# Kernel optimization log

Hardware: AMD Instinct MI355X
Metric: run time of the kernel (lower is better)

Reference implementation:

```python
import jax, jax.numpy as jnp
import numpy as np
from jax import lax

D = 1024      # hidden_dim
H = 1408      # moe_inter_dim
E = 8         # num_experts
K = 2         # topk
ROUTER_SCALE = 1.0


def setup_inputs() -> dict:
    key = jax.random.key(0)
    ks = jax.random.split(key, 16)
    s = 0.02
    inp = {
        "x": jax.random.normal(ks[0], (2, 2048, D), dtype=jnp.float32),
        "gate_w": jax.random.normal(ks[1], (E, D), dtype=jnp.float32) * s,
        "gate_b": jax.random.normal(ks[2], (E,), dtype=jnp.float32) * s,
        # stacked expert params; torch Linear weight [out,in] stored transposed as [in,out]
        "w1": jax.random.normal(ks[3], (E, D, H), dtype=jnp.float32) * s,
        "b1": jax.random.normal(ks[4], (E, H), dtype=jnp.float32) * s,
        "w3": jax.random.normal(ks[5], (E, D, H), dtype=jnp.float32) * s,
        "b3": jax.random.normal(ks[6], (E, H), dtype=jnp.float32) * s,
        "w2": jax.random.normal(ks[7], (E, H, D), dtype=jnp.float32) * s,
        "b2": jax.random.normal(ks[8], (E, D), dtype=jnp.float32) * s,
        # shared expert
        "sw1": jax.random.normal(ks[9], (D, H), dtype=jnp.float32) * s,
        "sb1": jax.random.normal(ks[10], (H,), dtype=jnp.float32) * s,
        "sw3": jax.random.normal(ks[11], (D, H), dtype=jnp.float32) * s,
        "sb3": jax.random.normal(ks[12], (H,), dtype=jnp.float32) * s,
        "sw2": jax.random.normal(ks[13], (H, D), dtype=jnp.float32) * s,
        "sb2": jax.random.normal(ks[14], (D,), dtype=jnp.float32) * s,
    }
    return inp


def _expert(x, w1, b1, w3, b3, w2, b2):
    # NOTE: source applies silu to the PRODUCT: w2(silu(w1(x) * w3(x)))
    h = jax.nn.silu((x @ w1 + b1) * (x @ w3 + b3))
    return h @ w2 + b2


def reference(x, gate_w, gate_b, w1, b1, w3, b3, w2, b2,
              sw1, sb1, sw3, sb3, sw2, sb2):
    shape = x.shape
    xf = x.reshape(-1, D)                      # [T, D]
    T = xf.shape[0]

    # Gate
    scores = jax.nn.softmax(xf @ gate_w.T, axis=-1)   # [T, E]
    biased = scores + gate_b
    _, idx = lax.top_k(biased, K)                     # [T, K] int32
    w = jnp.take_along_axis(scores, idx, axis=-1) * ROUTER_SCALE  # [T, K]

    # Dense routing-weight matrix (top-k indices are distinct per token)
    rw = jnp.zeros((T, E), dtype=xf.dtype).at[jnp.arange(T)[:, None], idx].add(w)

    # Stacked expert compute: [T, E, H] -> [T, E, D], combined by routing weight
    h = jax.nn.silu((jnp.einsum('td,edh->teh', xf, w1) + b1)
                    * (jnp.einsum('td,edh->teh', xf, w3) + b3))
    oe = jnp.einsum('teh,ehd->ted', h, w2) + b2
    y = jnp.einsum('te,ted->td', rw, oe)

    # Shared expert on all tokens
    z = _expert(xf, sw1, sb1, sw3, sb3, sw2, sb2)
    return (y + z).reshape(shape)
```

## Files before the change

### kernel.cpp

```cpp
#include <hip/hip_runtime.h>
#include <math.h>

#define DD 1024
#define HH 1408
#define NE 8

typedef __attribute__((ext_vector_type(8))) __bf16 bf16x8;
typedef __attribute__((ext_vector_type(4))) float f32x4;

__device__ __forceinline__ float bf2f(unsigned short u) {
  union { unsigned int i; float f; } v; v.i = ((unsigned int)u) << 16; return v.f;
}
__device__ __forceinline__ unsigned short f2bf(float f) {
  union { float f; unsigned int i; } v; v.f = f;
  unsigned int r = v.i + 0x7FFFu + ((v.i >> 16) & 1u);
  return (unsigned short)(r >> 16);
}
__device__ __forceinline__ float tof(float f) { return f; }
__device__ __forceinline__ float tof(unsigned short u) { return bf2f(u); }

__device__ __forceinline__ void cvt2(float a, float b, unsigned int* o) {
  asm("v_cvt_pk_bf16_f32 %0, %1, %2" : "=v"(*o) : "v"(a), "v"(b));
}

__device__ __forceinline__ void ld8cvt(const float* p, unsigned int* o) {
  float4 a = *(const float4*)p;
  float4 b = *(const float4*)(p + 4);
  cvt2(a.x, a.y, o + 0); cvt2(a.z, a.w, o + 1);
  cvt2(b.x, b.y, o + 2); cvt2(b.z, b.w, o + 3);
}

typedef unsigned int __attribute__((address_space(1))) gu32;
typedef unsigned int __attribute__((address_space(3))) lu32;
__device__ __forceinline__ void gl16(const unsigned short* g, unsigned short* l) {
  __builtin_amdgcn_global_load_lds((const gu32*)g, (lu32*)l, 16, 0, 0);
}

__global__ void sniff_kernel(const unsigned short* __restrict__ xw,
                             int* __restrict__ dflag) {
  __shared__ int cnt;
  if (threadIdx.x == 0) cnt = 0;
  __syncthreads();
  unsigned short v = xw[threadIdx.x];
  int e = (v >> 7) & 0xFF;
  if (e >= 100 && e <= 140) atomicAdd(&cnt, 1);
  __syncthreads();
  if (threadIdx.x == 0) dflag[0] = (cnt < 230) ? 1 : 0;
}

__global__ void cvtx_kernel(const void* __restrict__ x,
                            const int* __restrict__ dflag,
                            unsigned short* __restrict__ xb, int n8) {
  int i = blockIdx.x * blockDim.x + threadIdx.x;
  int st = gridDim.x * blockDim.x;
  if (dflag[0]) {
    const float* xs = (const float*)x;
    for (; i < n8; i += st) {
      unsigned int o[4];
      ld8cvt(xs + (size_t)i * 8, o);
      *(uint4*)(xb + (size_t)i * 8) = *(uint4*)o;
    }
  } else {
    const uint4* xs = (const uint4*)x;
    for (; i < n8; i += st) *(uint4*)(xb + (size_t)i * 8) = xs[i];
  }
}

__global__ void trans_kernel(const void* __restrict__ wmain,
                             const void* __restrict__ wsh,
                             const int* __restrict__ dflag,
                             unsigned short* __restrict__ out, int R, int C) {
  __shared__ float tile[32][33];
  const int mat = blockIdx.z;
  const int r0 = blockIdx.y << 5, c0 = blockIdx.x << 5;
  const int t = threadIdx.x;
  const int lr = t >> 3, lc = (t & 7) << 2;
  const size_t mbase = (size_t)mat * R * C;
  if (dflag[0]) {
    const float* src = (mat < NE) ? ((const float*)wmain + mbase) : (const float*)wsh;
    float4 v = *(const float4*)(src + (size_t)(r0 + lr) * C + c0 + lc);
    tile[lr][lc] = v.x; tile[lr][lc + 1] = v.y;
    tile[lr][lc + 2] = v.z; tile[lr][lc + 3] = v.w;
  } else {
    const unsigned short* src = (mat < NE) ? ((const unsigned short*)wmain + mbase)
                                           : (const unsigned short*)wsh;
    ushort4 v = *(const ushort4*)(src + (size_t)(r0 + lr) * C + c0 + lc);
    tile[lr][lc] = bf2f(v.x); tile[lr][lc + 1] = bf2f(v.y);
    tile[lr][lc + 2] = bf2f(v.z); tile[lr][lc + 3] = bf2f(v.w);
  }
  __syncthreads();
  const int oc = t >> 3;
  const int orr = (t & 7) << 2;
  unsigned int p0, p1;
  cvt2(tile[orr][oc], tile[orr + 1][oc], &p0);
  cvt2(tile[orr + 2][oc], tile[orr + 3][oc], &p1);
  uint2 pk; pk.x = p0; pk.y = p1;
  *(uint2*)(out + mbase + (size_t)(c0 + oc) * R + r0 + orr) = pk;
}

__global__ void cvtb_kernel(const void* b1, const void* b3, const void* b2,
                            const void* sb1, const void* sb3, const void* sb2,
                            const int* __restrict__ dflag,
                            float* __restrict__ bf1, float* __restrict__ bf3,
                            float* __restrict__ bf2o) {
  int i = blockIdx.x * blockDim.x + threadIdx.x;
  const int nh = (NE + 1) * HH, nd = (NE + 1) * DD;
  const bool f32 = dflag[0] != 0;
  auto get = [&](const void* pm, const void* ps, int idx, int per) -> float {
    int mat = idx / per, j = idx - mat * per;
    if (f32) return (mat < NE) ? ((const float*)pm)[(size_t)mat * per + j]
                               : ((const float*)ps)[j];
    return bf2f((mat < NE) ? ((const unsigned short*)pm)[(size_t)mat * per + j]
                           : ((const unsigned short*)ps)[j]);
  };
  if (i < nh) bf1[i] = get(b1, sb1, i, HH);
  else if (i < 2 * nh) bf3[i - nh] = get(b3, sb3, i - nh, HH);
  else if (i < 2 * nh + nd) bf2o[i - 2 * nh] = get(b2, sb2, i - 2 * nh, DD);
}

template <class T>
__device__ void gate_body(const T* __restrict__ x,
                          const T* __restrict__ gw,
                          const T* __restrict__ gb,
                          int* __restrict__ tok_eidx,
                          float* __restrict__ tok_w, int T_) {
  int t = (int)((blockIdx.x * blockDim.x + threadIdx.x) >> 6);
  int lane = threadIdx.x & 63;
  if (t >= T_) return;
  const T* xr = x + (size_t)t * DD;
  float acc[NE];
#pragma unroll
  for (int e = 0; e < NE; e++) acc[e] = 0.f;
  for (int i = lane; i < DD; i += 64) {
    float xv = tof(xr[i]);
#pragma unroll
    for (int e = 0; e < NE; e++) acc[e] += xv * tof(gw[e * DD + i]);
  }
#pragma unroll
  for (int off = 32; off > 0; off >>= 1) {
#pragma unroll
    for (int e = 0; e < NE; e++) acc[e] += __shfl_xor(acc[e], off);
  }
  if (lane == 0) {
    float mx = acc[0];
#pragma unroll
    for (int e = 1; e < NE; e++) mx = fmaxf(mx, acc[e]);
    float s = 0.f, sc[NE], bi[NE];
#pragma unroll
    for (int e = 0; e < NE; e++) { sc[e] = expf(acc[e] - mx); s += sc[e]; }
    float inv = 1.f / s;
#pragma unroll
    for (int e = 0; e < NE; e++) { sc[e] *= inv; bi[e] = sc[e] + tof(gb[e]); }
    int i1 = 0;
#pragma unroll
    for (int e = 1; e < NE; e++) if (bi[e] > bi[i1]) i1 = e;
    int i2 = (i1 == 0) ? 1 : 0;
#pragma unroll
    for (int e = 0; e < NE; e++) if (e != i1 && bi[e] > bi[i2]) i2 = e;
    tok_eidx[t * 2] = i1; tok_eidx[t * 2 + 1] = i2;
    tok_w[t * 2] = sc[i1]; tok_w[t * 2 + 1] = sc[i2];
  }
}

__global__ void gate_kernel(const void* x, const void* gw, const void* gb,
                            const int* __restrict__ dflag,
                            int* tok_eidx, float* tok_w, int T_) {
  if (dflag[0])
    gate_body<float>((const float*)x, (const float*)gw, (const float*)gb,
                     tok_eidx, tok_w, T_);
  else
    gate_body<unsigned short>((const unsigned short*)x, (const unsigned short*)gw,
                              (const unsigned short*)gb, tok_eidx, tok_w, T_);
}

__global__ void prep_kernel(const int* __restrict__ tok_eidx,
                            const float* __restrict__ tok_w,
                            int* __restrict__ meta,
                            int* __restrict__ rows_tok,
                            float* __restrict__ rows_wgt,
                            int t0, int TS) {
  __shared__ int cnt[NE];
  __shared__ int off[NE];
  const int tid = threadIdx.x;
  if (tid < NE) cnt[tid] = 0;
  __syncthreads();
  const int n2 = TS * 2;
  const int* te = tok_eidx + (size_t)t0 * 2;
  const float* tw = tok_w + (size_t)t0 * 2;
  for (int i = tid; i < n2; i += (int)blockDim.x) atomicAdd(&cnt[te[i]], 1);
  __syncthreads();
  if (tid == 0) {
    int s = 0;
#pragma unroll
    for (int e = 0; e < NE; e++) { off[e] = s; meta[16 + e] = s; s += cnt[e]; }
    meta[16 + NE] = s;
  }
  __syncthreads();
  for (int i = tid; i < n2; i += (int)blockDim.x) {
    int pos = atomicAdd(&off[te[i]], 1);
    rows_tok[pos] = t0 + (i >> 1);
    rows_wgt[pos] = tw[i];
  }
}

__global__ void zero_kernel(float4* __restrict__ p, int n4) {
  int i = blockIdx.x * blockDim.x + threadIdx.x;
  int st = gridDim.x * blockDim.x;
  float4 z; z.x = z.y = z.z = z.w = 0.f;
  for (; i < n4; i += st) p[i] = z;
}

__global__ __launch_bounds__(512, 2)
void ffn_up_kernel(const unsigned short* __restrict__ xb,
                   const unsigned short* __restrict__ wt1,
                   const unsigned short* __restrict__ wt3,
                   const float* __restrict__ bf1, const float* __restrict__ bf3,
                   const int* __restrict__ meta,
                   const int* __restrict__ rows_tok,
                   unsigned short* __restrict__ h_buf,
                   unsigned short* __restrict__ sh_buf,
                   int t0, int TS, int my) {
  const int NX = HH / 128;
  const int P = NX * (NE + 1);
  const int id = blockIdx.x;
  const int xcd = id & 7;
  const int rest = id >> 3;
  const int mtile = rest % my;
  const int chunk = rest / my;
  const int panel = chunk * 8 + xcd;
  if (panel >= P) return;
  const int z = panel / NX;
  const int n0 = (panel - z * NX) * 128;

  const bool shx = (z == NE);
  int g0, cnt;
  unsigned short* ho;
  if (shx) { g0 = 0; cnt = TS; ho = sh_buf; }
  else {
    g0 = meta[16 + z]; cnt = meta[17 + z] - g0;
    ho = h_buf + (size_t)g0 * HH;
  }
  if (mtile * 256 >= cnt) return;
  const unsigned short* wa = wt1 + (size_t)z * HH * DD;
  const unsigned short* wb = wt3 + (size_t)z * HH * DD;

  __shared__ alignas(16) unsigned short lds[2 * 32768];

  const int tid = threadIdx.x;
  const int lane = tid & 63, wid = tid >> 6;
  const int rsub = wid * 8 + (lane >> 3);
  const int sl8 = (((lane & 7) ^ (lane >> 3)) << 3);

  size_t aoff[4];
#pragma unroll
  for (int c = 0; c < 4; c++) {
    int r = c * 64 + rsub;
    int m = mtile * 256 + r;
    int rr = (m < cnt) ? m : (cnt - 1);
    int srow = shx ? (t0 + rr) : rows_tok[g0 + rr];
    aoff[c] = (size_t)srow * DD + sl8;
  }
  size_t boff[2];
#pragma unroll
  for (int c = 0; c < 2; c++)
    boff[c] = (size_t)(n0 + c * 64 + rsub) * DD + sl8;

  const int ln15 = lane & 15;
  const int lg = lane >> 4;
  const int wr = (wid >> 1) << 6;
  const int wc = (wid & 1) << 6;
  const int ldsw = wid * 512;

  f32x4 acc1[4][4], acc3[4][4];
#pragma unroll
  for (int a = 0; a < 4; a++)
#pragma unroll
    for (int b = 0; b < 4; b++) {
      acc1[a][b] = {0.f, 0.f, 0.f, 0.f};
      acc3[a][b] = {0.f, 0.f, 0.f, 0.f};
    }

  auto stage = [&](int buf, int k) {
    unsigned short* Lb = &lds[buf * 32768];
#pragma unroll
    for (int c = 0; c < 4; c++)
      gl16(xb + aoff[c] + k, Lb + c * 4096 + ldsw);
#pragma unroll
    for (int c = 0; c < 2; c++) {
      gl16(wa + boff[c] + k, Lb + 16384 + c * 4096 + ldsw);
      gl16(wb + boff[c] + k, Lb + 24576 + c * 4096 + ldsw);
    }
  };

  stage(0, 0);
  const int NT = DD / 64;
  for (int t = 0; t < NT; ++t) {
    asm volatile("s_waitcnt vmcnt(0)" ::: "memory");
    __syncthreads();
    if (t + 1 < NT) stage((t + 1) & 1, (t + 1) * 64);
    const unsigned short* Lb = &lds[(t & 1) * 32768];
#pragma unroll
    for (int ks = 0; ks < 2; ks++) {
      bf16x8 af[4];
#pragma unroll
      for (int fm = 0; fm < 4; fm++) {
        int R = wr + fm * 16 + ln15;
        af[fm] = *(const bf16x8*)&Lb[R * 64 + ((((ks << 2) | lg) ^ (R & 7)) << 3)];
      }
#pragma unroll
      for (int fn = 0; fn < 4; fn++) {
        int Rb = wc + fn * 16 + ln15;
        int o = Rb * 64 + ((((ks << 2) | lg) ^ (Rb & 7)) << 3);
        bf16x8 b1v = *(const bf16x8*)&Lb[16384 + o];
        bf16x8 b3v = *(const bf16x8*)&Lb[24576 + o];
#pragma unroll
        for (int fm = 0; fm < 4; fm++) {
          acc1[fm][fn] = __builtin_amdgcn_mfma_f32_16x16x32_bf16(af[fm], b1v, acc1[fm][fn], 0, 0, 0);
          acc3[fm][fn] = __builtin_amdgcn_mfma_f32_16x16x32_bf16(af[fm], b3v, acc3[fm][fn], 0, 0, 0);
        }
      }
    }
  }

  const int kq4 = lg << 2;
#pragma unroll
  for (int fm = 0; fm < 4; fm++) {
#pragma unroll
    for (int r = 0; r < 4; r++) {
      int m = mtile * 256 + wr + fm * 16 + kq4 + r;
      if (m < cnt) {
        unsigned short* orow = ho + (size_t)m * HH + n0;
#pragma unroll
        for (int fn = 0; fn < 4; fn++) {
          int nc = wc + fn * 16 + ln15;
          float g1 = acc1[fm][fn][r] + bf1[(size_t)z * HH + n0 + nc];
          float g3 = acc3[fm][fn][r] + bf3[(size_t)z * HH + n0 + nc];
          float u = g1 * g3;
          float hv = u * __builtin_amdgcn_rcpf(1.f + __expf(-u));
          orow[nc] = f2bf(hv);
        }
      }
    }
  }
}

__global__ __launch_bounds__(512, 2)
void ffn_down_kernel(const unsigned short* __restrict__ h_buf,
                     const unsigned short* __restrict__ sh_buf,
                     const unsigned short* __restrict__ wt2,
                     const float* __restrict__ bf2,
                     const int* __restrict__ meta,
                     const int* __restrict__ rows_tok,
                     const float* __restrict__ rows_wgt,
                     float* __restrict__ out, int t0, int TS, int my) {
  const int NX = DD / 128;
  const int P = NX * (NE + 1);
  const int id = blockIdx.x;
  const int xcd = id & 7;
  const int rest = id >> 3;
  const int mtile = rest % my;
  const int chunk = rest / my;
  const int panel = chunk * 8 + xcd;
  if (panel >= P) return;
  const int z = panel / NX;
  const int n0 = (panel - z * NX) * 128;

  const bool shx = (z == NE);
  int g0, cnt;
  const unsigned short* hb;
  if (shx) { g0 = 0; cnt = TS; hb = sh_buf; }
  else {
    g0 = meta[16 + z]; cnt = meta[17 + z] - g0;
    hb = h_buf + (size_t)g0 * HH;
  }
  if (mtile * 256 >= cnt) return;
  const unsigned short* ws = wt2 + (size_t)z * DD * HH;

  __shared__ alignas(16) unsigned short lds[2 * 24576];

  const int tid = threadIdx.x;
  const int lane = tid & 63, wid = tid >> 6;
  const int rsub = wid * 8 + (lane >> 3);
  const int sl8 = (((lane & 7) ^ (lane >> 3)) << 3);

  size_t aoff[4];
#pragma unroll
  for (int c = 0; c < 4; c++) {
    int r = c * 64 + rsub;
    int m = mtile * 256 + r;
    int rr = (m < cnt) ? m : (cnt - 1);
    aoff[c] = (size_t)rr * HH + sl8;
  }
  size_t boff[2];
#pragma unroll
  for (int c = 0; c < 2; c++)
    boff[c] = (size_t)(n0 + c * 64 + rsub) * HH + sl8;

  const int ln15 = lane & 15;
  const int lg = lane >> 4;
  const int wr = (wid >> 1) << 6;
  const int wc = (wid & 1) << 6;
  const int ldsw = wid * 512;

  f32x4 acc[4][4];
#pragma unroll
  for (int a = 0; a < 4; a++)
#pragma unroll
    for (int b = 0; b < 4; b++) acc[a][b] = {0.f, 0.f, 0.f, 0.f};

  auto stage = [&](int buf, int k) {
    unsigned short* Lb = &lds[buf * 24576];
#pragma unroll
    for (int c = 0; c < 4; c++)
      gl16(hb + aoff[c] + k, Lb + c * 4096 + ldsw);
#pragma unroll
    for (int c = 0; c < 2; c++)
      gl16(ws + boff[c] + k, Lb + 16384 + c * 4096 + ldsw);
  };

  stage(0, 0);
  const int NT = HH / 64;
  for (int t = 0; t < NT; ++t) {
    asm volatile("s_waitcnt vmcnt(0)" ::: "memory");
    __syncthreads();
    if (t + 1 < NT) stage((t + 1) & 1, (t + 1) * 64);
    const unsigned short* Lb = &lds[(t & 1) * 24576];
#pragma unroll
    for (int ks = 0; ks < 2; ks++) {
      bf16x8 af[4];
#pragma unroll
      for (int fm = 0; fm < 4; fm++) {
        int R = wr + fm * 16 + ln15;
        af[fm] = *(const bf16x8*)&Lb[R * 64 + ((((ks << 2) | lg) ^ (R & 7)) << 3)];
      }
#pragma unroll
      for (int fn = 0; fn < 4; fn++) {
        int Rb = wc + fn * 16 + ln15;
        int o = Rb * 64 + ((((ks << 2) | lg) ^ (Rb & 7)) << 3);
        bf16x8 bv = *(const bf16x8*)&Lb[16384 + o];
#pragma unroll
        for (int fm = 0; fm < 4; fm++)
          acc[fm][fn] = __builtin_amdgcn_mfma_f32_16x16x32_bf16(af[fm], bv, acc[fm][fn], 0, 0, 0);
      }
    }
  }

  const int kq4 = lg << 2;
#pragma unroll
  for (int fm = 0; fm < 4; fm++) {
#pragma unroll
    for (int r4 = 0; r4 < 4; r4++) {
      int m = mtile * 256 + wr + fm * 16 + kq4 + r4;
      if (m < cnt) {
        int t; float wgt;
        if (shx) { t = t0 + m; wgt = 1.f; }
        else { t = rows_tok[g0 + m]; wgt = rows_wgt[g0 + m]; }
        float* orow = out + (size_t)t * DD + n0;
#pragma unroll
        for (int fn = 0; fn < 4; fn++) {
          int nc = wc + fn * 16 + ln15;
          float v = wgt * (acc[fm][fn][r4] + bf2[(size_t)z * DD + n0 + nc]);
          atomicAdd(&orow[nc], v);
        }
      }
    }
  }
}

extern "C" void kernel_launch(void* const* d_in, const int* in_sizes, int n_in,
                              void* d_out, int out_size, void* d_ws, size_t ws_size,
                              hipStream_t stream) {
  const void* x   = d_in[0];
  const void* gw  = d_in[1];
  const void* gb  = d_in[2];
  const void* w1  = d_in[3];
  const void* b1  = d_in[4];
  const void* w3  = d_in[5];
  const void* b3  = d_in[6];
  const void* w2  = d_in[7];
  const void* b2  = d_in[8];
  const void* sw1 = d_in[9];
  const void* sb1 = d_in[10];
  const void* sw3 = d_in[11];
  const void* sb3 = d_in[12];
  const void* sw2 = d_in[13];
  const void* sb2 = d_in[14];

  const int T = in_sizes[0] / DD;
  (void)n_in; (void)out_size;

  const size_t WMAT = (size_t)(NE + 1) * HH * DD;

  auto need = [&](int S) -> size_t {
    int TS = T / S;
    size_t o = 0;
    auto pad = [&](size_t b) { o = (o + b + 255) & ~(size_t)255; };
    pad(256);
    pad(32 * sizeof(int));
    pad((size_t)T * 2 * sizeof(int));
    pad((size_t)T * 2 * sizeof(float));
    pad((size_t)T * DD * 2);
    pad(WMAT * 2);
    pad(WMAT * 2);
    pad(WMAT * 2);
    pad((size_t)(NE + 1) * HH * sizeof(float));
    pad((size_t)(NE + 1) * HH * sizeof(float));
    pad((size_t)(NE + 1) * DD * sizeof(float));
    pad((size_t)TS * 2 * sizeof(int));
    pad((size_t)TS * 2 * sizeof(float));
    pad((size_t)TS * 2 * HH * 2);
    pad((size_t)TS * HH * 2);
    return o;
  };
  int S = 32;
  {
    const int cand[6] = {1, 2, 4, 8, 16, 32};
    for (int ci = 0; ci < 6; ci++) {
      if (need(cand[ci]) <= ws_size) { S = cand[ci]; break; }
    }
  }
  const int TS = T / S;
  const int my = (TS + 255) / 256;

  char* w = (char*)d_ws;
  size_t off = 0;
  auto take = [&](size_t bytes) {
    char* p = w + off;
    off = (off + bytes + 255) & ~(size_t)255;
    return p;
  };
  int*   dflag    = (int*)  take(256);
  int*   meta     = (int*)  take(32 * sizeof(int));
  int*   tok_eidx = (int*)  take((size_t)T * 2 * sizeof(int));
  float* tok_w    = (float*)take((size_t)T * 2 * sizeof(float));
  unsigned short* xb  = (unsigned short*)take((size_t)T * DD * 2);
  unsigned short* wt1 = (unsigned short*)take(WMAT * 2);
  unsigned short* wt3 = (unsigned short*)take(WMAT * 2);
  unsigned short* wt2 = (unsigned short*)take(WMAT * 2);
  float* bf1 = (float*)take((size_t)(NE + 1) * HH * sizeof(float));
  float* bf3 = (float*)take((size_t)(NE + 1) * HH * sizeof(float));
  float* bf2 = (float*)take((size_t)(NE + 1) * DD * sizeof(float));
  int*   rows_tok = (int*)  take((size_t)TS * 2 * sizeof(int));
  float* rows_wgt = (float*)take((size_t)TS * 2 * sizeof(float));
  unsigned short* h_buf  = (unsigned short*)take((size_t)TS * 2 * HH * 2);
  unsigned short* sh_buf = (unsigned short*)take((size_t)TS * HH * 2);

  sniff_kernel<<<1, 256, 0, stream>>>((const unsigned short*)x, dflag);

  cvtx_kernel<<<2048, 256, 0, stream>>>(x, dflag, xb, T * DD / 8);
  trans_kernel<<<dim3(HH / 32, DD / 32, NE + 1), 256, 0, stream>>>(w1, sw1, dflag, wt1, DD, HH);
  trans_kernel<<<dim3(HH / 32, DD / 32, NE + 1), 256, 0, stream>>>(w3, sw3, dflag, wt3, DD, HH);
  trans_kernel<<<dim3(DD / 32, HH / 32, NE + 1), 256, 0, stream>>>(w2, sw2, dflag, wt2, HH, DD);
  {
    int nb = (2 * (NE + 1) * HH + (NE + 1) * DD + 255) / 256;
    cvtb_kernel<<<nb, 256, 0, stream>>>(b1, b3, b2, sb1, sb3, sb2, dflag, bf1, bf3, bf2);
  }

  gate_kernel<<<(T + 3) / 4, 256, 0, stream>>>(x, gw, gb, dflag, tok_eidx, tok_w, T);
  zero_kernel<<<1024, 256, 0, stream>>>((float4*)d_out, T * DD / 4);

  const int upP = (HH / 128) * (NE + 1);
  const int dnP = (DD / 128) * (NE + 1);
  const int upGrid = 8 * ((upP + 7) / 8) * my;
  const int dnGrid = 8 * ((dnP + 7) / 8) * my;

  for (int s = 0; s < S; s++) {
    const int t0 = s * TS;
    prep_kernel<<<1, 1024, 0, stream>>>(tok_eidx, tok_w, meta, rows_tok, rows_wgt, t0, TS);
    ffn_up_kernel<<<upGrid, 512, 0, stream>>>(
        xb, wt1, wt3, bf1, bf3, meta, rows_tok, h_buf, sh_buf, t0, TS, my);
    ffn_down_kernel<<<dnGrid, 512, 0, stream>>>(
        h_buf, sh_buf, wt2, bf2, meta, rows_tok, rows_wgt, (float*)d_out, t0, TS, my);
  }
}
```

Measured before the change: 455.7 us.

## Replace atomic scatter with per-row outputs plus combine, and overlap next-tile loads

The down-projection no longer scatters into the output with float atomics. Routed rows are written to a per-row buffer, the shared expert writes the output directly, and a new combine kernel gathers each token's two expert rows and adds them. That also makes the separate zero pass unnecessary. Both GEMM main loops now issue the next stage's global-to-LDS loads before waiting, using partial vmcnt, plus explicit barriers and setprio around the MFMA block, so loads overlap compute. This costs an extra fp32 buffer round trip and one more launch per slice.

```diff
diff --git a/kernel.cpp b/kernel.cpp
--- a/kernel.cpp
+++ b/kernel.cpp
@@ -178,6 +178,7 @@
                             int* __restrict__ meta,
                             int* __restrict__ rows_tok,
                             float* __restrict__ rows_wgt,
+                            int* __restrict__ tok_pos,
                             int t0, int TS) {
   __shared__ int cnt[NE];
   __shared__ int off[NE];
@@ -200,14 +201,28 @@
     int pos = atomicAdd(&off[te[i]], 1);
     rows_tok[pos] = t0 + (i >> 1);
     rows_wgt[pos] = tw[i];
-  }
-}
-
-__global__ void zero_kernel(float4* __restrict__ p, int n4) {
+    tok_pos[(size_t)(t0 + (i >> 1)) * 2 + (i & 1)] = pos;
+  }
+}
+
+__global__ void combine_kernel(const float4* __restrict__ r_out,
+                               const int* __restrict__ tok_pos,
+                               float4* __restrict__ out, int t0, int TS) {
+  const int C4 = DD / 4;
   int i = blockIdx.x * blockDim.x + threadIdx.x;
+  int n4 = TS * C4;
   int st = gridDim.x * blockDim.x;
-  float4 z; z.x = z.y = z.z = z.w = 0.f;
-  for (; i < n4; i += st) p[i] = z;
+  for (; i < n4; i += st) {
+    int tl = i / C4, c = i - tl * C4;
+    int t = t0 + tl;
+    int p0 = tok_pos[t * 2], p1 = tok_pos[t * 2 + 1];
+    float4 a = out[(size_t)t * C4 + c];
+    float4 b = r_out[(size_t)p0 * C4 + c];
+    float4 d = r_out[(size_t)p1 * C4 + c];
+    a.x += b.x + d.x; a.y += b.y + d.y;
+    a.z += b.z + d.z; a.w += b.w + d.w;
+    out[(size_t)t * C4 + c] = a;
+  }
 }
 
 __global__ __launch_bounds__(512, 2)
@@ -295,10 +310,17 @@
   stage(0, 0);
   const int NT = DD / 64;
   for (int t = 0; t < NT; ++t) {
-    asm volatile("s_waitcnt vmcnt(0)" ::: "memory");
-    __syncthreads();
-    if (t + 1 < NT) stage((t + 1) & 1, (t + 1) * 64);
+    if (t + 1 < NT) {
+      stage((t + 1) & 1, (t + 1) * 64);
+      asm volatile("s_waitcnt vmcnt(8)" ::: "memory");
+    } else {
+      asm volatile("s_waitcnt vmcnt(0)" ::: "memory");
+    }
+    __builtin_amdgcn_sched_barrier(0);
+    __builtin_amdgcn_s_barrier();
+    __builtin_amdgcn_sched_barrier(0);
     const unsigned short* Lb = &lds[(t & 1) * 32768];
+    __builtin_amdgcn_s_setprio(1);
 #pragma unroll
     for (int ks = 0; ks < 2; ks++) {
       bf16x8 af[4];
@@ -320,6 +342,11 @@
         }
       }
     }
+    __builtin_amdgcn_s_setprio(0);
+    asm volatile("s_waitcnt lgkmcnt(0)" ::: "memory");
+    __builtin_amdgcn_sched_barrier(0);
+    __builtin_amdgcn_s_barrier();
+    __builtin_amdgcn_sched_barrier(0);
   }
 
   const int kq4 = lg << 2;
@@ -352,6 +379,7 @@
                      const int* __restrict__ meta,
                      const int* __restrict__ rows_tok,
                      const float* __restrict__ rows_wgt,
+                     float* __restrict__ r_out,
                      float* __restrict__ out, int t0, int TS, int my) {
   const int NX = DD / 128;
   const int P = NX * (NE + 1);
@@ -421,10 +449,17 @@
   stage(0, 0);
   const int NT = HH / 64;
   for (int t = 0; t < NT; ++t) {
-    asm volatile("s_waitcnt vmcnt(0)" ::: "memory");
-    __syncthreads();
-    if (t + 1 < NT) stage((t + 1) & 1, (t + 1) * 64);
+    if (t + 1 < NT) {
+      stage((t + 1) & 1, (t + 1) * 64);
+      asm volatile("s_waitcnt vmcnt(6)" ::: "memory");
+    } else {
+      asm volatile("s_waitcnt vmcnt(0)" ::: "memory");
+    }
+    __builtin_amdgcn_sched_barrier(0);
+    __builtin_amdgcn_s_barrier();
+    __builtin_amdgcn_sched_barrier(0);
     const unsigned short* Lb = &lds[(t & 1) * 24576];
+    __builtin_amdgcn_s_setprio(1);
 #pragma unroll
     for (int ks = 0; ks < 2; ks++) {
       bf16x8 af[4];
@@ -443,6 +478,11 @@
           acc[fm][fn] = __builtin_amdgcn_mfma_f32_16x16x32_bf16(af[fm], bv, acc[fm][fn], 0, 0, 0);
       }
     }
+    __builtin_amdgcn_s_setprio(0);
+    asm volatile("s_waitcnt lgkmcnt(0)" ::: "memory");
+    __builtin_amdgcn_sched_barrier(0);
+    __builtin_amdgcn_s_barrier();
+    __builtin_amdgcn_sched_barrier(0);
   }
 
   const int kq4 = lg << 2;
@@ -452,15 +492,14 @@
     for (int r4 = 0; r4 < 4; r4++) {
       int m = mtile * 256 + wr + fm * 16 + kq4 + r4;
       if (m < cnt) {
-        int t; float wgt;
-        if (shx) { t = t0 + m; wgt = 1.f; }
-        else { t = rows_tok[g0 + m]; wgt = rows_wgt[g0 + m]; }
-        float* orow = out + (size_t)t * DD + n0;
+        float* orow;
+        float wgt;
+        if (shx) { orow = out + (size_t)(t0 + m) * DD + n0; wgt = 1.f; }
+        else { orow = r_out + (size_t)(g0 + m) * DD + n0; wgt = rows_wgt[g0 + m]; }
 #pragma unroll
         for (int fn = 0; fn < 4; fn++) {
           int nc = wc + fn * 16 + ln15;
-          float v = wgt * (acc[fm][fn][r4] + bf2[(size_t)z * DD + n0 + nc]);
-          atomicAdd(&orow[nc], v);
+          orow[nc] = wgt * (acc[fm][fn][r4] + bf2[(size_t)z * DD + n0 + nc]);
         }
       }
     }
@@ -499,6 +538,7 @@
     pad(32 * sizeof(int));
     pad((size_t)T * 2 * sizeof(int));
     pad((size_t)T * 2 * sizeof(float));
+    pad((size_t)T * 2 * sizeof(int));
     pad((size_t)T * DD * 2);
     pad(WMAT * 2);
     pad(WMAT * 2);
@@ -510,6 +550,7 @@
     pad((size_t)TS * 2 * sizeof(float));
     pad((size_t)TS * 2 * HH * 2);
     pad((size_t)TS * HH * 2);
+    pad((size_t)TS * 2 * DD * sizeof(float));
     return o;
   };
   int S = 32;
@@ -533,6 +574,7 @@
   int*   meta     = (int*)  take(32 * sizeof(int));
   int*   tok_eidx = (int*)  take((size_t)T * 2 * sizeof(int));
   float* tok_w    = (float*)take((size_t)T * 2 * sizeof(float));
+  int*   tok_pos  = (int*)  take((size_t)T * 2 * sizeof(int));
   unsigned short* xb  = (unsigned short*)take((size_t)T * DD * 2);
   unsigned short* wt1 = (unsigned short*)take(WMAT * 2);
   unsigned short* wt3 = (unsigned short*)take(WMAT * 2);
@@ -544,6 +586,7 @@
   float* rows_wgt = (float*)take((size_t)TS * 2 * sizeof(float));
   unsigned short* h_buf  = (unsigned short*)take((size_t)TS * 2 * HH * 2);
   unsigned short* sh_buf = (unsigned short*)take((size_t)TS * HH * 2);
+  float* r_out = (float*)take((size_t)TS * 2 * DD * sizeof(float));
 
   sniff_kernel<<<1, 256, 0, stream>>>((const unsigned short*)x, dflag);
 
@@ -557,7 +600,6 @@
   }
 
   gate_kernel<<<(T + 3) / 4, 256, 0, stream>>>(x, gw, gb, dflag, tok_eidx, tok_w, T);
-  zero_kernel<<<1024, 256, 0, stream>>>((float4*)d_out, T * DD / 4);
 
   const int upP = (HH / 128) * (NE + 1);
   const int dnP = (DD / 128) * (NE + 1);
@@ -566,10 +608,14 @@
 
   for (int s = 0; s < S; s++) {
     const int t0 = s * TS;
-    prep_kernel<<<1, 1024, 0, stream>>>(tok_eidx, tok_w, meta, rows_tok, rows_wgt, t0, TS);
+    prep_kernel<<<1, 1024, 0, stream>>>(tok_eidx, tok_w, meta, rows_tok, rows_wgt,
+                                        tok_pos, t0, TS);
     ffn_up_kernel<<<upGrid, 512, 0, stream>>>(
         xb, wt1, wt3, bf1, bf3, meta, rows_tok, h_buf, sh_buf, t0, TS, my);
     ffn_down_kernel<<<dnGrid, 512, 0, stream>>>(
-        h_buf, sh_buf, wt2, bf2, meta, rows_tok, rows_wgt, (float*)d_out, t0, TS, my);
-  }
-}
+        h_buf, sh_buf, wt2, bf2, meta, rows_tok, rows_wgt, r_out,
+        (float*)d_out, t0, TS, my);
+    combine_kernel<<<1024, 256, 0, stream>>>((const float4*)r_out, tok_pos,
+                                             (float4*)d_out, t0, TS);
+  }
+}
```

After: 454.5 us. Within noise of the previous version (-0.3%).
